# Kernel optimization log

Measured on AMD Instinct MI355X. Metric: run time of the kernel, lower is better.

## Reference

```python
import jax, jax.numpy as jnp
import numpy as np

N, D, K = 10000, 784, 16          # nodes, input feat dim, num_neighbors
E = N * (K - 1)                   # edges
H = 128                           # hidden width in all MLPs
SIZES = [784, 128, 2]             # node_sizes


def setup_inputs() -> dict:
    key = jax.random.key(0)
    ks = jax.random.split(key, 24)
    w = lambda k, shape: jax.random.normal(k, shape, jnp.float32) * 0.02
    inp = {
        "x": jax.random.normal(ks[0], (N, D), jnp.float32),
        "edge_attr": jax.random.uniform(ks[1], (E, 1), jnp.float32),
        "idxs": jax.random.randint(ks[2], (N, K - 1), 0, N, dtype=jnp.int32),
    }
    # Layer 1: in=784, msg_size=784, out=128
    inp["l1_msg_w1"] = w(ks[3], (D + 1, H));      inp["l1_msg_b1"] = jnp.zeros((H,), jnp.float32)
    inp["l1_msg_w2"] = w(ks[4], (H, D));          inp["l1_msg_b2"] = jnp.zeros((D,), jnp.float32)
    inp["l1_node_w1"] = w(ks[5], (D + D, H));     inp["l1_node_b1"] = jnp.zeros((H,), jnp.float32)
    inp["l1_node_w2"] = w(ks[6], (H, 128));       inp["l1_node_b2"] = jnp.zeros((128,), jnp.float32)
    # Layer 2: in=128, msg_size=128, out=2
    inp["l2_msg_w1"] = w(ks[7], (128 + 1, H));    inp["l2_msg_b1"] = jnp.zeros((H,), jnp.float32)
    inp["l2_msg_w2"] = w(ks[8], (H, 128));        inp["l2_msg_b2"] = jnp.zeros((128,), jnp.float32)
    inp["l2_node_w1"] = w(ks[9], (128 + 128, H)); inp["l2_node_b1"] = jnp.zeros((H,), jnp.float32)
    inp["l2_node_w2"] = w(ks[10], (H, 2));        inp["l2_node_b2"] = jnp.zeros((2,), jnp.float32)
    return inp


def _mlp(x, w1, b1, w2, b2):
    return jax.nn.relu(x @ w1 + b1) @ w2 + b2


def _node_layer(x, src, edge_attr,
                mw1, mb1, mw2, mb2, nw1, nb1, nw2, nb2):
    # message over edges: cat(x[src], edge_attr) -> MLP   [E, msg_size]
    msg = _mlp(jnp.concatenate([x[src], edge_attr], axis=1), mw1, mb1, mw2, mb2)
    # scatter_mean by src index (faithful to the original, which uses index=src)
    sums = jax.ops.segment_sum(msg, src, num_segments=N)
    cnt = jax.ops.segment_sum(jnp.ones((src.shape[0], 1), msg.dtype), src, num_segments=N)
    agg = jnp.where(cnt > 0, sums / jnp.maximum(cnt, 1.0), 0.0)
    # node update: cat(x, agg_msg) -> MLP
    return _mlp(jnp.concatenate([x, agg], axis=1), nw1, nb1, nw2, nb2)


def reference(x, edge_attr, idxs,
              l1_msg_w1, l1_msg_b1, l1_msg_w2, l1_msg_b2,
              l1_node_w1, l1_node_b1, l1_node_w2, l1_node_b2,
              l2_msg_w1, l2_msg_b1, l2_msg_w2, l2_msg_b2,
              l2_node_w1, l2_node_b1, l2_node_w2, l2_node_b2):
    src = idxs.reshape(-1)  # [E]; dst is unused by the original message computation
    h = _node_layer(x, src, edge_attr,
                    l1_msg_w1, l1_msg_b1, l1_msg_w2, l1_msg_b2,
                    l1_node_w1, l1_node_b1, l1_node_w2, l1_node_b2)
    proj = _node_layer(h, src, edge_attr,
                       l2_msg_w1, l2_msg_b1, l2_msg_w2, l2_msg_b2,
                       l2_node_w1, l2_node_b1, l2_node_w2, l2_node_b2)  # [N, 2]
    # vectorized per-neighbor squared distances (replaces the nested python loop)
    neigh = proj[idxs]                                   # [N, K-1, 2]
    d = jnp.sum((proj[:, None, :] - neigh) ** 2, axis=-1)  # [N, K-1]
    return d.reshape(-1, 1)                              # [N*(K-1), 1]
```

## Files before the change

kernel.cpp:

```cpp
#include <hip/hip_runtime.h>

#define N_NODES 10000
#define E_EDGES 150000
#define KNB     15
#define EBLOCKS 587
#define GEMMB   626
#define KPAD    832

typedef unsigned short u16;
typedef __bf16 bf16x8 __attribute__((ext_vector_type(8)));
typedef float  f32x4  __attribute__((ext_vector_type(4)));
typedef unsigned short u16x8 __attribute__((ext_vector_type(8)));

__device__ __forceinline__ void split3(float a, u16& h, u16& m, u16& l) {
    unsigned u = __float_as_uint(a);
    unsigned t = u + 0x7FFFu + ((u >> 16) & 1u);
    h = (u16)(t >> 16);
    float r1 = a - __uint_as_float(t & 0xFFFF0000u);
    unsigned u1 = __float_as_uint(r1);
    m = (u16)(u1 >> 16);
    float r2 = r1 - __uint_as_float(u1 & 0xFFFF0000u);
    l = (u16)(__float_as_uint(r2) >> 16);
}

__global__ void count_kernel(const int* __restrict__ idxs, int* __restrict__ cnt, int e) {
    int i = blockIdx.x * blockDim.x + threadIdx.x;
    if (i < e) atomicAdd(&cnt[idxs[i]], 1);
}

__device__ __forceinline__
void gemm_tile2(const float* __restrict__ A, int K,
                const float* __restrict__ Blo, const float* __restrict__ Bhi, int ldB,
                float* __restrict__ C, int ldC, int M,
                int rowBlk, int colBlk) {
    __shared__ float As2[16][34];
    __shared__ float Bs2[16][64];
    int tid = threadIdx.x;
    int tn  = tid & 15, tm = tid >> 4;
    int arow = tid >> 3, acB = (tid & 7) << 1;
    int brow = tid >> 4, bcol = (tid & 15) << 2;
    int rowBase = rowBlk * 32, colBase = colBlk * 64;

    bool half = (Bhi != nullptr) && (colBase >= 128);
    const float* B = half ? Bhi : Blo;
    int bj = colBase - (half ? 128 : 0) + bcol;

    float2 av; float4 bv;
    auto loadA = [&](int k0, float2& dst) {
        int gr = rowBase + arow;
        if (gr < M) dst = *(const float2*)(A + (size_t)gr * K + k0 + acB);
        else { dst.x = dst.y = 0.f; }
    };
    auto loadB = [&](int k0, float4& dst) {
        dst = *(const float4*)(B + (size_t)(k0 + brow) * ldB + bj);
    };
    loadA(0, av); loadB(0, bv);

    float acc[2][4] = {};
    for (int k0 = 0; k0 < K; k0 += 16) {
        __syncthreads();
        As2[acB + 0][arow] = av.x; As2[acB + 1][arow] = av.y;
        *(float4*)&Bs2[brow][bcol] = bv;
        __syncthreads();
        if (k0 + 16 < K) { loadA(k0 + 16, av); loadB(k0 + 16, bv); }
#pragma unroll
        for (int k = 0; k < 16; ++k) {
            float4 b = *(const float4*)&Bs2[k][tn << 2];
            float2 a = *(const float2*)&As2[k][tm << 1];
            acc[0][0] = fmaf(a.x, b.x, acc[0][0]); acc[0][1] = fmaf(a.x, b.y, acc[0][1]);
            acc[0][2] = fmaf(a.x, b.z, acc[0][2]); acc[0][3] = fmaf(a.x, b.w, acc[0][3]);
            acc[1][0] = fmaf(a.y, b.x, acc[1][0]); acc[1][1] = fmaf(a.y, b.y, acc[1][1]);
            acc[1][2] = fmaf(a.y, b.z, acc[1][2]); acc[1][3] = fmaf(a.y, b.w, acc[1][3]);
        }
    }
#pragma unroll
    for (int i = 0; i < 2; ++i) {
        int row = rowBase + tm * 2 + i;
        if (row >= M) continue;
#pragma unroll
        for (int j = 0; j < 4; ++j)
            C[(size_t)row * ldC + colBase + (tn << 2) + j] = acc[i][j];
    }
}

__global__ __launch_bounds__(256)
void scanfold_kernel(const float* __restrict__ mw2, const float* __restrict__ mb2,
                     const float* __restrict__ nw1, const float* __restrict__ nb2,
                     const float* __restrict__ nw2,
                     const float* __restrict__ m2w1, const float* __restrict__ m2b1,
                     const float* __restrict__ m2w2, const float* __restrict__ m2b2,
                     const float* __restrict__ n2w1, const float* __restrict__ n2b1,
                     float* __restrict__ M1, float* __restrict__ M2,
                     float* __restrict__ WH,
                     float* __restrict__ v1, float* __restrict__ v2,
                     float* __restrict__ bu2, float* __restrict__ bx2,
                     const int* __restrict__ cnt, int* __restrict__ eoff,
                     float* __restrict__ maskv, int* __restrict__ fillc,
                     const float* __restrict__ mw1, u16* __restrict__ Bt) {
    int b = blockIdx.x;
    if (b >= 41) {
        __shared__ float Lt[KPAD][17];
        int b2 = b - 41;
        int colBase = b2 * 16;
        const float* S = (colBase < 128) ? mw1 : nw1;
        int sc = colBase & 127;
        int tid = threadIdx.x;
        for (int i = 0; i < 52; ++i) {
            int row = (tid >> 4) + i * 16;
            Lt[row][tid & 15] = (row < 784) ? S[(size_t)row * 128 + sc + (tid & 15)] : 0.f;
        }
        __syncthreads();
        int col = tid >> 4, o = tid & 15;
        size_t dbase = (size_t)(colBase + col) * KPAD;
        for (int o2 = o; o2 < 104; o2 += 16) {
            u16 hs[8], ms[8], ls[8];
#pragma unroll
            for (int e = 0; e < 8; ++e) split3(Lt[o2 * 8 + e][col], hs[e], ms[e], ls[e]);
            auto pk = [](const u16* s) {
                uint4 v;
                v.x = s[0] | ((unsigned)s[1] << 16); v.y = s[2] | ((unsigned)s[3] << 16);
                v.z = s[4] | ((unsigned)s[5] << 16); v.w = s[6] | ((unsigned)s[7] << 16);
                return v;
            };
            *(uint4*)(Bt +          dbase + o2 * 8) = pk(hs);
            *(uint4*)(Bt + 212992 + dbase + o2 * 8) = pk(ms);
            *(uint4*)(Bt + 425984 + dbase + o2 * 8) = pk(ls);
        }
        return;
    }
    if (b == 0) {
        __shared__ int ssum[256];
        int tid = threadIdx.x;
        const int CH = 40;
        int base = tid * CH;
        int v[CH]; int s = 0;
#pragma unroll
        for (int q = 0; q < CH; ++q) {
            int i = base + q;
            v[q] = (i < N_NODES) ? cnt[i] : 0;
            s += v[q];
        }
        ssum[tid] = s;
        __syncthreads();
        for (int off = 1; off < 256; off <<= 1) {
            int t = (tid >= off) ? ssum[tid - off] : 0;
            __syncthreads();
            ssum[tid] += t;
            __syncthreads();
        }
        int ex = ssum[tid] - s;
#pragma unroll
        for (int q = 0; q < CH; ++q) {
            int i = base + q;
            if (i < N_NODES) {
                eoff[i]  = ex;
                maskv[i] = (v[q] > 0) ? 1.f : 0.f;
                fillc[i] = 0;
                ex += v[q];
            }
        }
        return;
    }
    b -= 1;
    if (b < 8) {
        gemm_tile2(mw2, 784, nw1 + 784 * 128, nullptr, 128, M1, 128, 128, b >> 1, b & 1);
    } else if (b < 16) {
        int t = b - 8;
        gemm_tile2(m2w2, 128, n2w1 + 128 * 128, nullptr, 128, M2, 128, 128, t >> 1, t & 1);
    } else if (b < 32) {
        int t = b - 16;
        gemm_tile2(nw2, 128, m2w1, n2w1, 128, WH, 256, 128, t >> 2, t & 3);
    } else {
        __shared__ float red[256];
        int t  = (b - 32) >> 1;
        int j  = ((b - 32) & 1) * 64 + (threadIdx.x & 63);
        int kq = threadIdx.x >> 6;
        const float* bvec; const float* Bv; const float* add; float* out; int Kv;
        if (t == 0)      { bvec = mb2;  Bv = nw1 + 784 * 128;  add = nullptr; out = v1;  Kv = 784; }
        else if (t == 1) { bvec = m2b2; Bv = n2w1 + 128 * 128; add = nullptr; out = v2;  Kv = 128; }
        else if (t == 2) { bvec = nb2;  Bv = m2w1;             add = m2b1;    out = bu2; Kv = 128; }
        else             { bvec = nb2;  Bv = n2w1;             add = n2b1;    out = bx2; Kv = 128; }
        float acc = 0.f;
        for (int k = kq; k < Kv; k += 4) acc = fmaf(bvec[k], Bv[k * 128 + j], acc);
        red[threadIdx.x] = acc;
        __syncthreads();
        if (threadIdx.x < 64) {
            float tot = red[threadIdx.x] + red[threadIdx.x + 64] +
                        red[threadIdx.x + 128] + red[threadIdx.x + 192];
            out[j] = tot + (add ? add[j] : 0.f);
        }
    }
}

#define MF(a, b, c) __builtin_amdgcn_mfma_f32_16x16x32_bf16((a), (b), (c), 0, 0, 0)

__device__ __forceinline__
void gemm_mfma(const float* __restrict__ A, const u16* __restrict__ Bt,
               const float* __restrict__ biasLo, const float* __restrict__ biasHi,
               const float* __restrict__ vhi, const float* __restrict__ rowmask,
               float* __restrict__ C, int gb) {
    __shared__ u16 Bs[3][2][8][64][8];
    __shared__ u16 As[3][2][2][64][8];
    const int tid  = threadIdx.x;
    const int lane = tid & 63, w = tid >> 6;
    const int rb = gb >> 1, cb = gb & 1;
    const int rowBase = rb * 32, colBase = cb * 128;
    u16* const AsB = &As[0][0][0][0][0];
    u16* const BsB = &Bs[0][0][0][0][0];

    const int r   = tid >> 3;
    const int oct = tid & 7;
    const int aoff = oct << 3;
    int arow = rowBase + r; if (arow > N_NODES - 1) arow = N_NODES - 1;
    const float* Ap = A + (size_t)arow * 784;
    u16* aDst = AsB + (oct >> 2) * 1024 + (r >> 4) * 512 + (((r & 15) + ((oct & 3) << 4)) << 3);

#define BDEF(j) \
    const int c_##j = w * 12 + j; \
    const int pl##j = c_##j >> 4, kt##j = (c_##j >> 3) & 1, cf##j = c_##j & 7; \
    const int bofs##j = pl##j * 212992 + (colBase + cf##j * 16 + (lane & 15)) * KPAD \
                        + kt##j * 32 + ((lane >> 4) << 3); \
    const int bd##j = (((pl##j * 2 + kt##j) * 8 + cf##j) << 9) + (lane << 3); \
    uint4 bv##j;
    BDEF(0) BDEF(1) BDEF(2) BDEF(3) BDEF(4) BDEF(5)
    BDEF(6) BDEF(7) BDEF(8) BDEF(9) BDEF(10) BDEF(11)
#undef BDEF

    float4 av0, av1;
    u16x8 a3h, a3m, a3l;

#define ALOAD(k0) { int kk = (k0) + aoff; \
    if (kk < 784) { av0 = *(const float4*)(Ap + kk); av1 = *(const float4*)(Ap + kk + 4); } \
    else { av0.x=av0.y=av0.z=av0.w=0.f; av1 = av0; } }
#define BLOADALL(k0) \
    bv0  = *(const uint4*)(Bt + bofs0  + (k0)); \
    bv1  = *(const uint4*)(Bt + bofs1  + (k0)); \
    bv2  = *(const uint4*)(Bt + bofs2  + (k0)); \
    bv3  = *(const uint4*)(Bt + bofs3  + (k0)); \
    bv4  = *(const uint4*)(Bt + bofs4  + (k0)); \
    bv5  = *(const uint4*)(Bt + bofs5  + (k0)); \
    bv6  = *(const uint4*)(Bt + bofs6  + (k0)); \
    bv7  = *(const uint4*)(Bt + bofs7  + (k0)); \
    bv8  = *(const uint4*)(Bt + bofs8  + (k0)); \
    bv9  = *(const uint4*)(Bt + bofs9  + (k0)); \
    bv10 = *(const uint4*)(Bt + bofs10 + (k0)); \
    bv11 = *(const uint4*)(Bt + bofs11 + (k0));
#define ASPLIT() { u16 h, m, l; \
    split3(av0.x, h, m, l); a3h[0] = h; a3m[0] = m; a3l[0] = l; \
    split3(av0.y, h, m, l); a3h[1] = h; a3m[1] = m; a3l[1] = l; \
    split3(av0.z, h, m, l); a3h[2] = h; a3m[2] = m; a3l[2] = l; \
    split3(av0.w, h, m, l); a3h[3] = h; a3m[3] = m; a3l[3] = l; \
    split3(av1.x, h, m, l); a3h[4] = h; a3m[4] = m; a3l[4] = l; \
    split3(av1.y, h, m, l); a3h[5] = h; a3m[5] = m; a3l[5] = l; \
    split3(av1.z, h, m, l); a3h[6] = h; a3m[6] = m; a3l[6] = l; \
    split3(av1.w, h, m, l); a3h[7] = h; a3m[7] = m; a3l[7] = l; }

    f32x4 acc00 = {0.f, 0.f, 0.f, 0.f};
    f32x4 acc01 = acc00, acc10 = acc00, acc11 = acc00;

    ALOAD(0) BLOADALL(0) ASPLIT()

    const u16* aFr = AsB + (lane << 3);
    const u16* bFr = BsB + ((w * 2) << 9) + (lane << 3);

#define KTBLOCK(KT) { \
    bf16x8 a0h = *(const bf16x8*)(aFr + (KT)*1024); \
    bf16x8 a1h = *(const bf16x8*)(aFr + (KT)*1024 + 512); \
    bf16x8 a0m = *(const bf16x8*)(aFr + (KT)*1024 + 2048); \
    bf16x8 a1m = *(const bf16x8*)(aFr + (KT)*1024 + 2560); \
    bf16x8 a0l = *(const bf16x8*)(aFr + (KT)*1024 + 4096); \
    bf16x8 a1l = *(const bf16x8*)(aFr + (KT)*1024 + 4608); \
    bf16x8 bb0 = *(const bf16x8*)(bFr + (KT)*4096); \
    bf16x8 bb1 = *(const bf16x8*)(bFr + (KT)*4096 + 512); \
    acc00 = MF(a0h, bb0, acc00); acc01 = MF(a0h, bb1, acc01); \
    acc10 = MF(a1h, bb0, acc10); acc11 = MF(a1h, bb1, acc11); \
    acc00 = MF(a0m, bb0, acc00); acc01 = MF(a0m, bb1, acc01); \
    acc10 = MF(a1m, bb0, acc10); acc11 = MF(a1m, bb1, acc11); \
    acc00 = MF(a0l, bb0, acc00); acc01 = MF(a0l, bb1, acc01); \
    acc10 = MF(a1l, bb0, acc10); acc11 = MF(a1l, bb1, acc11); \
    bf16x8 bc0 = *(const bf16x8*)(bFr + (KT)*4096 + 8192); \
    bf16x8 bc1 = *(const bf16x8*)(bFr + (KT)*4096 + 8704); \
    acc00 = MF(a0h, bc0, acc00); acc01 = MF(a0h, bc1, acc01); \
    acc10 = MF(a1h, bc0, acc10); acc11 = MF(a1h, bc1, acc11); \
    acc00 = MF(a0m, bc0, acc00); acc01 = MF(a0m, bc1, acc01); \
    acc10 = MF(a1m, bc0, acc10); acc11 = MF(a1m, bc1, acc11); \
    bf16x8 be0 = *(const bf16x8*)(bFr + (KT)*4096 + 16384); \
    bf16x8 be1 = *(const bf16x8*)(bFr + (KT)*4096 + 16896); \
    acc00 = MF(a0h, be0, acc00); acc01 = MF(a0h, be1, acc01); \
    acc10 = MF(a1h, be0, acc10); acc11 = MF(a1h, be1, acc11); }

    for (int t = 0; t < 13; ++t) {
        __syncthreads();
        *(u16x8*)(aDst)        = a3h;
        *(u16x8*)(aDst + 2048) = a3m;
        *(u16x8*)(aDst + 4096) = a3l;
        *(uint4*)(BsB + bd0)  = bv0;
        *(uint4*)(BsB + bd1)  = bv1;
        *(uint4*)(BsB + bd2)  = bv2;
        *(uint4*)(BsB + bd3)  = bv3;
        *(uint4*)(BsB + bd4)  = bv4;
        *(uint4*)(BsB + bd5)  = bv5;
        *(uint4*)(BsB + bd6)  = bv6;
        *(uint4*)(BsB + bd7)  = bv7;
        *(uint4*)(BsB + bd8)  = bv8;
        *(uint4*)(BsB + bd9)  = bv9;
        *(uint4*)(BsB + bd10) = bv10;
        *(uint4*)(BsB + bd11) = bv11;
        __syncthreads();
        const int kn = (t + 1) << 6;
        if (t < 12) { ALOAD(kn) BLOADALL(kn) }
        KTBLOCK(0)
        KTBLOCK(1)
        if (t < 12) ASPLIT()
    }
#undef ALOAD
#undef BLOADALL
#undef ASPLIT
#undef KTBLOCK

    const float* bias = cb ? biasHi : biasLo;
#define EPI(rf, cf, ACC) { \
        const int col = colBase + w * 32 + (cf) * 16 + (lane & 15); \
        const int cj  = col & 127; \
        const float bb = bias[cj]; \
        const float vh = cb ? vhi[cj] : 0.f; \
        const int rbase = rowBase + (rf) * 16 + ((lane >> 4) << 2); \
        _Pragma("unroll") \
        for (int rr = 0; rr < 4; ++rr) { \
            int row = rbase + rr; \
            if (row < N_NODES) { \
                float v = ACC[rr] + bb; \
                if (cb) v = fmaf(rowmask[row], vh, v); \
                C[(size_t)row * 256 + col] = v; \
            } } }
    EPI(0, 0, acc00) EPI(0, 1, acc01) EPI(1, 0, acc10) EPI(1, 1, acc11)
#undef EPI
}

__global__ __launch_bounds__(256)
void fillgemm_kernel(const int* __restrict__ idxs, const float* __restrict__ ea,
                     const int* __restrict__ eoff, int* __restrict__ fillc,
                     float* __restrict__ eas,
                     const float* __restrict__ A, const u16* __restrict__ Bt,
                     const float* __restrict__ biasLo, const float* __restrict__ biasHi,
                     const float* __restrict__ vhi, const float* __restrict__ rowmask,
                     float* __restrict__ C) {
    int gb = blockIdx.x;
    if (gb < GEMMB) {
        gemm_mfma(A, Bt, biasLo, biasHi, vhi, rowmask, C, gb);
        return;
    }
    int i = (gb - GEMMB) * 256 + threadIdx.x;
    if (i < E_EDGES) {
        int s = idxs[i];
        int p = atomicAdd(&fillc[s], 1);
        eas[eoff[s] + p] = ea[i];
    }
}

__global__ __launch_bounds__(512, 4)
void tail16_kernel(const float* __restrict__ UX1, const float* __restrict__ w1last,
                   const float* __restrict__ eas, const int* __restrict__ eoff,
                   const int* __restrict__ cnt, const float* __restrict__ maskv,
                   const float* __restrict__ M1, const float* __restrict__ WH,
                   const float* __restrict__ bu2, const float* __restrict__ bx2,
                   const float* __restrict__ v2,
                   const float* __restrict__ w2last, const float* __restrict__ M2,
                   const float* __restrict__ pw, const float* __restrict__ pb,
                   float* __restrict__ UX2, float* __restrict__ proj) {
    __shared__ float Bs[16][264];
    __shared__ float mhT[128][18];
    __shared__ float ts[16][132];
    __shared__ float ebuf[1024];
    int rowBase = blockIdx.x * 16;
    int tid = threadIdx.x;
    int tr  = tid >> 5;
    int tn  = tid & 31;
    int c4  = tn << 2;

    auto msg_phase = [&](const float* __restrict__ U, const float* __restrict__ wl) {
        int d = tid & 127, grp = tid >> 7;
        float w = wl[d];
        float uu[4], sum[4];
        int es[4], ec[4];
#pragma unroll
        for (int it = 0; it < 4; ++it) {
            int n  = rowBase + it * 4 + grp;
            ec[it] = cnt[n];
            es[it] = eoff[n];
            uu[it] = U[(size_t)n * 256 + d];
            sum[it] = 0.f;
        }
        int ebase = eoff[rowBase];
        int eend  = (rowBase + 16 < N_NODES) ? eoff[rowBase + 16] : E_EDGES;
        for (int w0 = ebase; w0 < eend; w0 += 1024) {
            int wlen = min(1024, eend - w0);
            __syncthreads();
            for (int q = tid; q < wlen; q += 512) ebuf[q] = eas[w0 + q];
            __syncthreads();
#pragma unroll
            for (int it = 0; it < 4; ++it) {
                int lo = max(es[it], w0), hiE = min(es[it] + ec[it], w0 + wlen);
                for (int e = lo; e < hiE; ++e)
                    sum[it] += fmaxf(fmaf(ebuf[e - w0], w, uu[it]), 0.f);
            }
        }
#pragma unroll
        for (int it = 0; it < 4; ++it)
            mhT[d][it * 4 + grp] = (ec[it] > 0) ? sum[it] / (float)ec[it] : 0.f;
    };

    msg_phase(UX1, w1last);

    {
        float a0 = 0.f, a1 = 0.f, a2 = 0.f, a3 = 0.f;
        float4 bv = *(const float4*)(M1 + (size_t)tr * 128 + c4);
        for (int k0 = 0; k0 < 128; k0 += 16) {
            __syncthreads();
            *(float4*)&Bs[tr][c4] = bv;
            __syncthreads();
            if (k0 + 16 < 128)
                bv = *(const float4*)(M1 + (size_t)(k0 + 16 + tr) * 128 + c4);
#pragma unroll
            for (int k = 0; k < 16; ++k) {
                float a = mhT[k0 + k][tr];
                float4 b = *(const float4*)&Bs[k][c4];
                a0 = fmaf(a, b.x, a0); a1 = fmaf(a, b.y, a1);
                a2 = fmaf(a, b.z, a2); a3 = fmaf(a, b.w, a3);
            }
        }
        int row = rowBase + tr;
        float4 xn = *(const float4*)(UX1 + (size_t)row * 256 + 128 + c4);
        float4 o;
        o.x = fmaxf(a0 + xn.x, 0.f);
        o.y = fmaxf(a1 + xn.y, 0.f);
        o.z = fmaxf(a2 + xn.z, 0.f);
        o.w = fmaxf(a3 + xn.w, 0.f);
        *(float4*)&ts[tr][c4] = o;
    }

    {
        float u0 = 0.f, u1 = 0.f, u2 = 0.f, u3 = 0.f;
        float x0 = 0.f, x1 = 0.f, x2 = 0.f, x3 = 0.f;
        int c8 = tn << 3;
        float4 bva = *(const float4*)(WH + (size_t)tr * 256 + c8);
        float4 bvb = *(const float4*)(WH + (size_t)tr * 256 + c8 + 4);
        for (int k0 = 0; k0 < 128; k0 += 16) {
            __syncthreads();
            *(float4*)&Bs[tr][c8]     = bva;
            *(float4*)&Bs[tr][c8 + 4] = bvb;
            __syncthreads();
            if (k0 + 16 < 128) {
                bva = *(const float4*)(WH + (size_t)(k0 + 16 + tr) * 256 + c8);
                bvb = *(const float4*)(WH + (size_t)(k0 + 16 + tr) * 256 + c8 + 4);
            }
#pragma unroll
            for (int k = 0; k < 16; ++k) {
                float a = ts[tr][k0 + k];
                float4 b0 = *(const float4*)&Bs[k][c4];
                float4 b1 = *(const float4*)&Bs[k][c4 + 128];
                u0 = fmaf(a, b0.x, u0); u1 = fmaf(a, b0.y, u1);
                u2 = fmaf(a, b0.z, u2); u3 = fmaf(a, b0.w, u3);
                x0 = fmaf(a, b1.x, x0); x1 = fmaf(a, b1.y, x1);
                x2 = fmaf(a, b1.z, x2); x3 = fmaf(a, b1.w, x3);
            }
        }
        int row = rowBase + tr;
        float rm = maskv[row];
        float4 o0, o1;
        o0.x = u0 + bu2[c4 + 0]; o0.y = u1 + bu2[c4 + 1];
        o0.z = u2 + bu2[c4 + 2]; o0.w = u3 + bu2[c4 + 3];
        o1.x = fmaf(rm, v2[c4 + 0], x0 + bx2[c4 + 0]);
        o1.y = fmaf(rm, v2[c4 + 1], x1 + bx2[c4 + 1]);
        o1.z = fmaf(rm, v2[c4 + 2], x2 + bx2[c4 + 2]);
        o1.w = fmaf(rm, v2[c4 + 3], x3 + bx2[c4 + 3]);
        float* orow = UX2 + (size_t)row * 256;
        *(float4*)(orow + c4)       = o0;
        *(float4*)(orow + 128 + c4) = o1;
    }
    __syncthreads();

    msg_phase(UX2, w2last);

    {
        float a0 = 0.f, a1 = 0.f, a2 = 0.f, a3 = 0.f;
        float4 bv = *(const float4*)(M2 + (size_t)tr * 128 + c4);
        for (int k0 = 0; k0 < 128; k0 += 16) {
            __syncthreads();
            *(float4*)&Bs[tr][c4] = bv;
            __syncthreads();
            if (k0 + 16 < 128)
                bv = *(const float4*)(M2 + (size_t)(k0 + 16 + tr) * 128 + c4);
#pragma unroll
            for (int k = 0; k < 16; ++k) {
                float a = mhT[k0 + k][tr];
                float4 b = *(const float4*)&Bs[k][c4];
                a0 = fmaf(a, b.x, a0); a1 = fmaf(a, b.y, a1);
                a2 = fmaf(a, b.z, a2); a3 = fmaf(a, b.w, a3);
            }
        }
        int row = rowBase + tr;
        float4 xn = *(const float4*)(UX2 + (size_t)row * 256 + 128 + c4);
        float t0 = fmaxf(a0 + xn.x, 0.f);
        float t1 = fmaxf(a1 + xn.y, 0.f);
        float t2 = fmaxf(a2 + xn.z, 0.f);
        float t3 = fmaxf(a3 + xn.w, 0.f);
        float pp0 = fmaf(t3, pw[2*(c4+3)],   fmaf(t2, pw[2*(c4+2)],   fmaf(t1, pw[2*(c4+1)],   t0 * pw[2*c4])));
        float pp1 = fmaf(t3, pw[2*(c4+3)+1], fmaf(t2, pw[2*(c4+2)+1], fmaf(t1, pw[2*(c4+1)+1], t0 * pw[2*c4+1])));
        for (int off = 16; off > 0; off >>= 1) {
            pp0 += __shfl_xor(pp0, off, 64);
            pp1 += __shfl_xor(pp1, off, 64);
        }
        if (tn == 0) {
            proj[2 * row]     = pp0 + pb[0];
            proj[2 * row + 1] = pp1 + pb[1];
        }
    }
}

__global__ void dist_kernel(const float* __restrict__ proj, const int* __restrict__ idxs,
                            float* __restrict__ out, int e) {
    int i = blockIdx.x * blockDim.x + threadIdx.x;
    if (i >= e) return;
    int n = i / KNB;
    int m = idxs[i];
    float2 pn = *(const float2*)(proj + 2 * n);
    float2 pm = *(const float2*)(proj + 2 * m);
    float dx = pn.x - pm.x;
    float dy = pn.y - pm.y;
    out[i] = dx * dx + dy * dy;
}

extern "C" void kernel_launch(void* const* d_in, const int* in_sizes, int n_in,
                              void* d_out, int out_size, void* d_ws, size_t ws_size,
                              hipStream_t stream) {
    (void)in_sizes; (void)n_in; (void)out_size; (void)ws_size;
    const float* x    = (const float*)d_in[0];
    const float* eatt = (const float*)d_in[1];
    const int*   idxs = (const int*)d_in[2];
    const float* mw1  = (const float*)d_in[3];
    const float* mb1  = (const float*)d_in[4];
    const float* mw2  = (const float*)d_in[5];
    const float* mb2  = (const float*)d_in[6];
    const float* nw1  = (const float*)d_in[7];
    const float* nb1  = (const float*)d_in[8];
    const float* nw2  = (const float*)d_in[9];
    const float* nb2  = (const float*)d_in[10];
    const float* m2w1 = (const float*)d_in[11];
    const float* m2b1 = (const float*)d_in[12];
    const float* m2w2 = (const float*)d_in[13];
    const float* m2b2 = (const float*)d_in[14];
    const float* n2w1 = (const float*)d_in[15];
    const float* n2b1 = (const float*)d_in[16];
    const float* n2w2 = (const float*)d_in[17];
    const float* n2b2 = (const float*)d_in[18];
    float* out = (float*)d_out;

    float* fws   = (float*)d_ws;
    float* UX1   = fws;
    float* UX2   = fws + 2560000;
    float* proj  = fws + 5120000;
    float* maskv = fws + 5140000;
    float* eas   = fws + 5150016;
    float* M1    = fws + 5300016;
    float* M2    = fws + 5316400;
    float* WH    = fws + 5332784;
    float* v1    = fws + 5365552;
    float* v2    = fws + 5365680;
    float* bu2   = fws + 5365808;
    float* bx2   = fws + 5365936;
    int*   cnt   = (int*)(fws + 5366064);
    int*   fillc = cnt + N_NODES;
    int*   eoff  = fillc + N_NODES;
    u16*   Bt    = (u16*)(fws + 2560000);

    hipMemsetAsync(cnt, 0, N_NODES * sizeof(int), stream);
    count_kernel<<<EBLOCKS, 256, 0, stream>>>(idxs, cnt, E_EDGES);

    scanfold_kernel<<<57, 256, 0, stream>>>(mw2, mb2, nw1, nb2, nw2,
                                            m2w1, m2b1, m2w2, m2b2, n2w1, n2b1,
                                            M1, M2, WH, v1, v2, bu2, bx2,
                                            cnt, eoff, maskv, fillc, mw1, Bt);

    fillgemm_kernel<<<GEMMB + EBLOCKS, 256, 0, stream>>>(
        idxs, eatt, eoff, fillc, eas,
        x, Bt, mb1, nb1, v1, maskv, UX1);

    tail16_kernel<<<625, 512, 0, stream>>>(UX1, mw1 + 784 * 128, eas, eoff, cnt, maskv,
                                           M1, WH, bu2, bx2, v2,
                                           m2w1 + 128 * 128, M2,
                                           n2w2, n2b2,
                                           UX2, proj);

    dist_kernel<<<EBLOCKS, 256, 0, stream>>>(proj, idxs, out, E_EDGES);
}
```

Measured before the change: 262.1 us.

## Load B fragments directly from global memory instead of staging through LDS

The GEMM no longer stages the pre-split bf16 weight planes (B) in shared memory. Each wave now reads its own MFMA B fragments straight from global memory every k-step, and the A-tile staging thread mapping is remapped so the fragment layout lines up. This removes the B LDS writes and reads and shrinks LDS use, but the B loads are now issued without prefetch, so their latency sits right before the MFMAs, and each B element is fetched redundantly by the blocks that share it (relying on cache).

```diff
diff --git a/kernel.cpp b/kernel.cpp
--- a/kernel.cpp
+++ b/kernel.cpp
@@ -6,6 +6,8 @@
 #define EBLOCKS 587
 #define GEMMB   626
 #define KPAD    832
+#define PLSTR   212992
+#define CFSTR   13312
 
 typedef unsigned short u16;
 typedef __bf16 bf16x8 __attribute__((ext_vector_type(8)));
@@ -122,9 +124,9 @@
                 v.z = s[4] | ((unsigned)s[5] << 16); v.w = s[6] | ((unsigned)s[7] << 16);
                 return v;
             };
-            *(uint4*)(Bt +          dbase + o2 * 8) = pk(hs);
-            *(uint4*)(Bt + 212992 + dbase + o2 * 8) = pk(ms);
-            *(uint4*)(Bt + 425984 + dbase + o2 * 8) = pk(ls);
+            *(uint4*)(Bt +           dbase + o2 * 8) = pk(hs);
+            *(uint4*)(Bt + PLSTR   + dbase + o2 * 8) = pk(ms);
+            *(uint4*)(Bt + 2*PLSTR + dbase + o2 * 8) = pk(ls);
         }
         return;
     }
@@ -199,32 +201,22 @@
                const float* __restrict__ biasLo, const float* __restrict__ biasHi,
                const float* __restrict__ vhi, const float* __restrict__ rowmask,
                float* __restrict__ C, int gb) {
-    __shared__ u16 Bs[3][2][8][64][8];
     __shared__ u16 As[3][2][2][64][8];
     const int tid  = threadIdx.x;
     const int lane = tid & 63, w = tid >> 6;
     const int rb = gb >> 1, cb = gb & 1;
     const int rowBase = rb * 32, colBase = cb * 128;
     u16* const AsB = &As[0][0][0][0][0];
-    u16* const BsB = &Bs[0][0][0][0][0];
-
-    const int r   = tid >> 3;
-    const int oct = tid & 7;
-    const int aoff = oct << 3;
-    int arow = rowBase + r; if (arow > N_NODES - 1) arow = N_NODES - 1;
+
+    const int skt = w >> 1, srf = w & 1;
+    const int aoff = skt * 32 + ((lane >> 4) << 3);
+    int arow = rowBase + srf * 16 + (lane & 15);
+    if (arow > N_NODES - 1) arow = N_NODES - 1;
     const float* Ap = A + (size_t)arow * 784;
-    u16* aDst = AsB + (oct >> 2) * 1024 + (r >> 4) * 512 + (((r & 15) + ((oct & 3) << 4)) << 3);
-
-#define BDEF(j) \
-    const int c_##j = w * 12 + j; \
-    const int pl##j = c_##j >> 4, kt##j = (c_##j >> 3) & 1, cf##j = c_##j & 7; \
-    const int bofs##j = pl##j * 212992 + (colBase + cf##j * 16 + (lane & 15)) * KPAD \
-                        + kt##j * 32 + ((lane >> 4) << 3); \
-    const int bd##j = (((pl##j * 2 + kt##j) * 8 + cf##j) << 9) + (lane << 3); \
-    uint4 bv##j;
-    BDEF(0) BDEF(1) BDEF(2) BDEF(3) BDEF(4) BDEF(5)
-    BDEF(6) BDEF(7) BDEF(8) BDEF(9) BDEF(10) BDEF(11)
-#undef BDEF
+    u16* aDst = AsB + skt * 1024 + srf * 512 + (lane << 3);
+
+    const u16* Bp = Bt + (size_t)(colBase + w * 32 + (lane & 15)) * KPAD
+                       + ((lane >> 4) << 3);
 
     float4 av0, av1;
     u16x8 a3h, a3m, a3l;
@@ -232,19 +224,6 @@
 #define ALOAD(k0) { int kk = (k0) + aoff; \
     if (kk < 784) { av0 = *(const float4*)(Ap + kk); av1 = *(const float4*)(Ap + kk + 4); } \
     else { av0.x=av0.y=av0.z=av0.w=0.f; av1 = av0; } }
-#define BLOADALL(k0) \
-    bv0  = *(const uint4*)(Bt + bofs0  + (k0)); \
-    bv1  = *(const uint4*)(Bt + bofs1  + (k0)); \
-    bv2  = *(const uint4*)(Bt + bofs2  + (k0)); \
-    bv3  = *(const uint4*)(Bt + bofs3  + (k0)); \
-    bv4  = *(const uint4*)(Bt + bofs4  + (k0)); \
-    bv5  = *(const uint4*)(Bt + bofs5  + (k0)); \
-    bv6  = *(const uint4*)(Bt + bofs6  + (k0)); \
-    bv7  = *(const uint4*)(Bt + bofs7  + (k0)); \
-    bv8  = *(const uint4*)(Bt + bofs8  + (k0)); \
-    bv9  = *(const uint4*)(Bt + bofs9  + (k0)); \
-    bv10 = *(const uint4*)(Bt + bofs10 + (k0)); \
-    bv11 = *(const uint4*)(Bt + bofs11 + (k0));
 #define ASPLIT() { u16 h, m, l; \
     split3(av0.x, h, m, l); a3h[0] = h; a3m[0] = m; a3l[0] = l; \
     split3(av0.y, h, m, l); a3h[1] = h; a3m[1] = m; a3l[1] = l; \
@@ -258,65 +237,75 @@
     f32x4 acc00 = {0.f, 0.f, 0.f, 0.f};
     f32x4 acc01 = acc00, acc10 = acc00, acc11 = acc00;
 
-    ALOAD(0) BLOADALL(0) ASPLIT()
+    ALOAD(0) ASPLIT()
 
     const u16* aFr = AsB + (lane << 3);
-    const u16* bFr = BsB + ((w * 2) << 9) + (lane << 3);
-
-#define KTBLOCK(KT) { \
-    bf16x8 a0h = *(const bf16x8*)(aFr + (KT)*1024); \
-    bf16x8 a1h = *(const bf16x8*)(aFr + (KT)*1024 + 512); \
-    bf16x8 a0m = *(const bf16x8*)(aFr + (KT)*1024 + 2048); \
-    bf16x8 a1m = *(const bf16x8*)(aFr + (KT)*1024 + 2560); \
-    bf16x8 a0l = *(const bf16x8*)(aFr + (KT)*1024 + 4096); \
-    bf16x8 a1l = *(const bf16x8*)(aFr + (KT)*1024 + 4608); \
-    bf16x8 bb0 = *(const bf16x8*)(bFr + (KT)*4096); \
-    bf16x8 bb1 = *(const bf16x8*)(bFr + (KT)*4096 + 512); \
-    acc00 = MF(a0h, bb0, acc00); acc01 = MF(a0h, bb1, acc01); \
-    acc10 = MF(a1h, bb0, acc10); acc11 = MF(a1h, bb1, acc11); \
-    acc00 = MF(a0m, bb0, acc00); acc01 = MF(a0m, bb1, acc01); \
-    acc10 = MF(a1m, bb0, acc10); acc11 = MF(a1m, bb1, acc11); \
-    acc00 = MF(a0l, bb0, acc00); acc01 = MF(a0l, bb1, acc01); \
-    acc10 = MF(a1l, bb0, acc10); acc11 = MF(a1l, bb1, acc11); \
-    bf16x8 bc0 = *(const bf16x8*)(bFr + (KT)*4096 + 8192); \
-    bf16x8 bc1 = *(const bf16x8*)(bFr + (KT)*4096 + 8704); \
-    acc00 = MF(a0h, bc0, acc00); acc01 = MF(a0h, bc1, acc01); \
-    acc10 = MF(a1h, bc0, acc10); acc11 = MF(a1h, bc1, acc11); \
-    acc00 = MF(a0m, bc0, acc00); acc01 = MF(a0m, bc1, acc01); \
-    acc10 = MF(a1m, bc0, acc10); acc11 = MF(a1m, bc1, acc11); \
-    bf16x8 be0 = *(const bf16x8*)(bFr + (KT)*4096 + 16384); \
-    bf16x8 be1 = *(const bf16x8*)(bFr + (KT)*4096 + 16896); \
-    acc00 = MF(a0h, be0, acc00); acc01 = MF(a0h, be1, acc01); \
-    acc10 = MF(a1h, be0, acc10); acc11 = MF(a1h, be1, acc11); }
 
     for (int t = 0; t < 13; ++t) {
         __syncthreads();
         *(u16x8*)(aDst)        = a3h;
         *(u16x8*)(aDst + 2048) = a3m;
         *(u16x8*)(aDst + 4096) = a3l;
-        *(uint4*)(BsB + bd0)  = bv0;
-        *(uint4*)(BsB + bd1)  = bv1;
-        *(uint4*)(BsB + bd2)  = bv2;
-        *(uint4*)(BsB + bd3)  = bv3;
-        *(uint4*)(BsB + bd4)  = bv4;
-        *(uint4*)(BsB + bd5)  = bv5;
-        *(uint4*)(BsB + bd6)  = bv6;
-        *(uint4*)(BsB + bd7)  = bv7;
-        *(uint4*)(BsB + bd8)  = bv8;
-        *(uint4*)(BsB + bd9)  = bv9;
-        *(uint4*)(BsB + bd10) = bv10;
-        *(uint4*)(BsB + bd11) = bv11;
-        __syncthreads();
-        const int kn = (t + 1) << 6;
-        if (t < 12) { ALOAD(kn) BLOADALL(kn) }
-        KTBLOCK(0)
-        KTBLOCK(1)
+        __syncthreads();
+        const int k0 = t << 6;
+        bf16x8 bh00 = *(const bf16x8*)(Bp + k0);
+        bf16x8 bh01 = *(const bf16x8*)(Bp + k0 + CFSTR);
+        bf16x8 bh10 = *(const bf16x8*)(Bp + k0 + 32);
+        bf16x8 bh11 = *(const bf16x8*)(Bp + k0 + CFSTR + 32);
+        bf16x8 bm00 = *(const bf16x8*)(Bp + k0 + PLSTR);
+        bf16x8 bm01 = *(const bf16x8*)(Bp + k0 + PLSTR + CFSTR);
+        bf16x8 bm10 = *(const bf16x8*)(Bp + k0 + PLSTR + 32);
+        bf16x8 bm11 = *(const bf16x8*)(Bp + k0 + PLSTR + CFSTR + 32);
+        bf16x8 bl00 = *(const bf16x8*)(Bp + k0 + 2*PLSTR);
+        bf16x8 bl01 = *(const bf16x8*)(Bp + k0 + 2*PLSTR + CFSTR);
+        bf16x8 bl10 = *(const bf16x8*)(Bp + k0 + 2*PLSTR + 32);
+        bf16x8 bl11 = *(const bf16x8*)(Bp + k0 + 2*PLSTR + CFSTR + 32);
+        if (t < 12) ALOAD((t + 1) << 6)
+
+        {
+            bf16x8 a0h = *(const bf16x8*)(aFr);
+            bf16x8 a1h = *(const bf16x8*)(aFr + 512);
+            bf16x8 a0m = *(const bf16x8*)(aFr + 2048);
+            bf16x8 a1m = *(const bf16x8*)(aFr + 2560);
+            bf16x8 a0l = *(const bf16x8*)(aFr + 4096);
+            bf16x8 a1l = *(const bf16x8*)(aFr + 4608);
+            acc00 = MF(a0h, bh00, acc00); acc01 = MF(a0h, bh01, acc01);
+            acc10 = MF(a1h, bh00, acc10); acc11 = MF(a1h, bh01, acc11);
+            acc00 = MF(a0m, bh00, acc00); acc01 = MF(a0m, bh01, acc01);
+            acc10 = MF(a1m, bh00, acc10); acc11 = MF(a1m, bh01, acc11);
+            acc00 = MF(a0l, bh00, acc00); acc01 = MF(a0l, bh01, acc01);
+            acc10 = MF(a1l, bh00, acc10); acc11 = MF(a1l, bh01, acc11);
+            acc00 = MF(a0h, bm00, acc00); acc01 = MF(a0h, bm01, acc01);
+            acc10 = MF(a1h, bm00, acc10); acc11 = MF(a1h, bm01, acc11);
+            acc00 = MF(a0m, bm00, acc00); acc01 = MF(a0m, bm01, acc01);
+            acc10 = MF(a1m, bm00, acc10); acc11 = MF(a1m, bm01, acc11);
+            acc00 = MF(a0h, bl00, acc00); acc01 = MF(a0h, bl01, acc01);
+            acc10 = MF(a1h, bl00, acc10); acc11 = MF(a1h, bl01, acc11);
+        }
+        {
+            bf16x8 a0h = *(const bf16x8*)(aFr + 1024);
+            bf16x8 a1h = *(const bf16x8*)(aFr + 1536);
+            bf16x8 a0m = *(const bf16x8*)(aFr + 3072);
+            bf16x8 a1m = *(const bf16x8*)(aFr + 3584);
+            bf16x8 a0l = *(const bf16x8*)(aFr + 5120);
+            bf16x8 a1l = *(const bf16x8*)(aFr + 5632);
+            acc00 = MF(a0h, bh10, acc00); acc01 = MF(a0h, bh11, acc01);
+            acc10 = MF(a1h, bh10, acc10); acc11 = MF(a1h, bh11, acc11);
+            acc00 = MF(a0m, bh10, acc00); acc01 = MF(a0m, bh11, acc01);
+            acc10 = MF(a1m, bh10, acc10); acc11 = MF(a1m, bh11, acc11);
+            acc00 = MF(a0l, bh10, acc00); acc01 = MF(a0l, bh11, acc01);
+            acc10 = MF(a1l, bh10, acc10); acc11 = MF(a1l, bh11, acc11);
+            acc00 = MF(a0h, bm10, acc00); acc01 = MF(a0h, bm11, acc01);
+            acc10 = MF(a1h, bm10, acc10); acc11 = MF(a1h, bm11, acc11);
+            acc00 = MF(a0m, bm10, acc00); acc01 = MF(a0m, bm11, acc01);
+            acc10 = MF(a1m, bm10, acc10); acc11 = MF(a1m, bm11, acc11);
+            acc00 = MF(a0h, bl10, acc00); acc01 = MF(a0h, bl11, acc01);
+            acc10 = MF(a1h, bl10, acc10); acc11 = MF(a1h, bl11, acc11);
+        }
         if (t < 12) ASPLIT()
     }
 #undef ALOAD
-#undef BLOADALL
 #undef ASPLIT
-#undef KTBLOCK
 
     const float* bias = cb ? biasHi : biasLo;
 #define EPI(rf, cf, ACC) { \
```

Measured after the change: 258.7 us. About the same (-1.3%).
